# Optimization experiments

Measured on AMD Instinct MI355X. Metric: run time of the kernel, lower is better.

## Reference

```python
import jax, jax.numpy as jnp
import numpy as np

NUM_CLASSES = 91
BBOX_XFORM_CLIP = float(np.log(1000.0 / 16.0))
WX, WY, WW, WH = 10.0, 10.0, 5.0, 5.0  # torchvision BoxCoder weights
DETECTIONS_PER_IMG = 100


def _decode_boxes(reg, props):
    # reg: [P, 4*C], props: [P, 4] -> [P, C, 4]  (torchvision BoxCoder.decode)
    widths = props[:, 2] - props[:, 0]
    heights = props[:, 3] - props[:, 1]
    ctr_x = props[:, 0] + 0.5 * widths
    ctr_y = props[:, 1] + 0.5 * heights
    r = reg.reshape(reg.shape[0], -1, 4)
    dx = r[..., 0] / WX
    dy = r[..., 1] / WY
    dw = jnp.minimum(r[..., 2] / WW, BBOX_XFORM_CLIP)
    dh = jnp.minimum(r[..., 3] / WH, BBOX_XFORM_CLIP)
    pcx = dx * widths[:, None] + ctr_x[:, None]
    pcy = dy * heights[:, None] + ctr_y[:, None]
    pw = jnp.exp(dw) * widths[:, None]
    ph = jnp.exp(dh) * heights[:, None]
    return jnp.stack([pcx - 0.5 * pw, pcy - 0.5 * ph, pcx + 0.5 * pw, pcy + 0.5 * ph], axis=-1)


def _clip_boxes(boxes, h, w):
    x = jnp.clip(boxes[..., 0::2], 0.0, float(w))
    y = jnp.clip(boxes[..., 1::2], 0.0, float(h))
    return jnp.stack([x[..., 0], y[..., 0], x[..., 1], y[..., 1]], axis=-1)


def setup_inputs() -> dict:
    key = jax.random.key(0)
    k1, k2, k3, k4, k5 = jax.random.split(key, 5)
    B, P, C, FD = 8, 4096, NUM_CLASSES, 1024
    N = B * P
    class_logits = jax.random.normal(k1, (N, C), dtype=jnp.float32)
    box_regression = 0.5 * jax.random.normal(k2, (N, 4 * C), dtype=jnp.float32)
    # valid proposal boxes inside an 800x800 image: x1<x2, y1<y2
    xy = jax.random.uniform(k3, (N, 2), dtype=jnp.float32) * 700.0
    wh = jax.random.uniform(k4, (N, 2), dtype=jnp.float32) * 96.0 + 4.0
    proposals = jnp.concatenate([xy, xy + wh], axis=-1)
    box_features = jax.random.normal(k5, (N, FD), dtype=jnp.float32)
    return {"class_logits": class_logits, "box_regression": box_regression,
            "proposals": proposals, "box_features": box_features,
            "batch_size": B, "image_h": 800, "image_w": 800}


def reference(class_logits, box_regression, proposals, box_features, batch_size, image_h, image_w):
    B = int(batch_size)
    N = class_logits.shape[0]
    P = N // B
    lg = class_logits.reshape(B, P, NUM_CLASSES)
    rg = box_regression.reshape(B, P, 4 * NUM_CLASSES)
    pr = proposals.reshape(B, P, 4)
    ft = box_features.reshape(B, P, -1)

    def per_image(lg_i, rg_i, pr_i, ft_i):
        boxes = _decode_boxes(rg_i, pr_i)            # [P, C, 4]
        scores = jax.nn.softmax(lg_i, axis=-1)       # [P, C]
        boxes = _clip_boxes(boxes, image_h, image_w)
        boxes = boxes[:, 1:].reshape(-1, 4)          # drop background class -> [P*(C-1), 4]
        scores = scores[:, 1:].reshape(-1)
        # batched_nms with iou_threshold=1.0 never suppresses anything (IoU<=1 always),
        # so keep == indices sorted by score descending, truncated to detections_per_img.
        keep = jnp.argsort(-scores)[:DETECTIONS_PER_IMG]
        boxes = boxes / float(image_h)               # source divides by image_shape[0] only
        kept_boxes = boxes[keep]                     # [D, 4]
        feat_idx = keep // (NUM_CLASSES - 1)         # source: keep / (num_classes-1) int div
        kept_feats = ft_i[feat_idx]                  # [D, FD]
        return kept_boxes, kept_feats

    all_boxes, all_features = jax.vmap(per_image)(lg, rg, pr, ft)
    return all_boxes, all_features
```

## Files before the change

### kernel.cpp

```cpp
#include <hip/hip_runtime.h>
#include <hip/hip_bf16.h>

#define NCLS 91
#define NFG 90
#define NDET 100
#define FDIM 1024
#define CAP 4096
#define NBUK 4096
#define PMAX 4096
#define BBOX_CLIP 4.135166556742356f
#define K1_TPB 256
#define RPB 32
#define K2_TPB 1024

__global__ __launch_bounds__(K1_TPB) void k1_soft(
        const float* __restrict__ logits, float* __restrict__ rowoff,
        unsigned* __restrict__ maxk, int N) {
    int wave = threadIdx.x >> 6, lane = threadIdx.x & 63;
    int rowbase = blockIdx.x * RPB + wave * (RPB / 4);
    for (int it = 0; it < RPB / 4; it++) {
        long long row = rowbase + it;
        if (row >= N) return;
        const float* r = logits + row * NCLS;
        float l1 = r[lane];
        float l2 = (lane < NCLS - 64) ? r[64 + lane] : -INFINITY;
        float m = fmaxf(l1, l2);
        #pragma unroll
        for (int o = 32; o; o >>= 1) m = fmaxf(m, __shfl_xor(m, o));
        float e = expf(l1 - m) + ((lane < NCLS - 64) ? expf(l2 - m) : 0.0f);
        #pragma unroll
        for (int o = 32; o; o >>= 1) e += __shfl_xor(e, o);
        float off = m + logf(e);
        unsigned ka = (lane >= 1) ? __float_as_uint(expf(l1 - off)) : 0u;
        unsigned kb = (lane < NCLS - 64) ? __float_as_uint(expf(l2 - off)) : 0u;
        unsigned km = ka > kb ? ka : kb;
        #pragma unroll
        for (int o = 32; o; o >>= 1) { unsigned t = __shfl_xor(km, o); km = km > t ? km : t; }
        if (lane == 0) { rowoff[row] = off; maxk[row] = km; }
    }
}

__global__ __launch_bounds__(K2_TPB) void k2_select(
        const float* __restrict__ logits, const float* __restrict__ reg,
        const float* __restrict__ props,
        const int* __restrict__ pH, const int* __restrict__ pW,
        const float* __restrict__ rowoff, const unsigned* __restrict__ maxk,
        float* __restrict__ outBoxes, unsigned* __restrict__ keepRow, int P) {
    __shared__ unsigned long long cand[CAP];
    __shared__ unsigned hist[NBUK];
    __shared__ unsigned hot[PMAX];
    __shared__ unsigned tpart[256];
    __shared__ unsigned tsuf[257];
    __shared__ unsigned keepR[NDET];
    __shared__ unsigned sh_lb, sh_nhot, sh_ncand;

    const int img = blockIdx.x;
    const int tid = threadIdx.x;
    const unsigned* mk = maxk + (size_t)img * P;

    if (tid == 0) { sh_nhot = 0; sh_ncand = 0; sh_lb = 0; }
    for (int b = tid; b < NBUK; b += K2_TPB) hist[b] = 0u;
    __syncthreads();

    for (int r = tid; r < P; r += K2_TPB) atomicAdd(&hist[mk[r] >> 20], 1u);
    __syncthreads();

    unsigned local[16];
    if (tid < 256) {
        unsigned s = 0;
        #pragma unroll
        for (int i = 0; i < 16; i++) { local[i] = hist[tid * 16 + i]; s += local[i]; }
        tpart[tid] = s;
    }
    __syncthreads();
    if (tid == 0) {
        unsigned run = 0; tsuf[256] = 0;
        for (int t = 255; t >= 0; t--) { run += tpart[t]; tsuf[t] = run; }
    }
    __syncthreads();
    if (tid < 256) {
        unsigned run = tsuf[tid + 1];
        #pragma unroll
        for (int i = 15; i >= 0; i--) {
            unsigned prev = run; run += local[i];
            if (run >= NDET && prev < NDET) sh_lb = ((unsigned)(tid * 16 + i)) << 20;
        }
    }
    __syncthreads();
    const unsigned lb = sh_lb;

    for (int r = tid; r < P; r += K2_TPB)
        if (mk[r] >= lb) hot[atomicAdd(&sh_nhot, 1u)] = (unsigned)r;
    __syncthreads();
    const int nhot = (int)sh_nhot;

    const int wave = tid >> 6, lane = tid & 63;
    for (int i = wave; i < nhot; i += K2_TPB / 64) {
        int rl = (int)hot[i];
        long long row = (long long)img * P + rl;
        float off = rowoff[row];
        const float* r = logits + row * NCLS;
        float l1 = r[lane];
        float l2 = (lane < NCLS - 64) ? r[64 + lane] : -INFINITY;
        if (lane >= 1) {
            unsigned k = __float_as_uint(expf(l1 - off));
            if (k >= lb) {
                unsigned pos = atomicAdd(&sh_ncand, 1u);
                if (pos < CAP)
                    cand[pos] = ((unsigned long long)k << 32) |
                                (unsigned)(0xFFFFFFFFu - (unsigned)(rl * NFG + lane - 1));
            }
        }
        if (lane < NCLS - 64) {
            unsigned k = __float_as_uint(expf(l2 - off));
            if (k >= lb) {
                unsigned pos = atomicAdd(&sh_ncand, 1u);
                if (pos < CAP)
                    cand[pos] = ((unsigned long long)k << 32) |
                                (unsigned)(0xFFFFFFFFu - (unsigned)(rl * NFG + 63 + lane));
            }
        }
    }
    __syncthreads();
    unsigned cnt = sh_ncand; if (cnt > CAP) cnt = CAP;

    int n = 128; while (n < (int)cnt) n <<= 1;
    for (int i = tid; i < n; i += K2_TPB) if (i >= (int)cnt) cand[i] = 0ULL;
    __syncthreads();
    for (int k = 2; k <= n; k <<= 1) {
        for (int j = k >> 1; j > 0; j >>= 1) {
            for (int i = tid; i < n; i += K2_TPB) {
                int ixj = i ^ j;
                if (ixj > i) {
                    bool up = ((i & k) == 0);
                    unsigned long long a = cand[i], b = cand[ixj];
                    if ((a > b) == up) { cand[i] = b; cand[ixj] = a; }
                }
            }
            __syncthreads();
        }
    }

    if (tid < NDET) {
        unsigned long long key = cand[n - 1 - tid];
        unsigned e = 0xFFFFFFFFu - (unsigned)(key & 0xFFFFFFFFull);
        int pr = e / NFG, cm = e - pr * NFG, c = cm + 1;
        long long rw = (long long)img * P + pr;
        float x1 = props[rw * 4 + 0], y1 = props[rw * 4 + 1];
        float x2 = props[rw * 4 + 2], y2 = props[rw * 4 + 3];
        float w = x2 - x1, hgt = y2 - y1;
        float cx = x1 + 0.5f * w, cy = y1 + 0.5f * hgt;
        const float* rr = reg + rw * (4 * NCLS) + 4 * c;
        float dx = rr[0] / 10.0f, dy = rr[1] / 10.0f;
        float dw = fminf(rr[2] / 5.0f, BBOX_CLIP);
        float dh = fminf(rr[3] / 5.0f, BBOX_CLIP);
        float pcx = dx * w + cx, pcy = dy * hgt + cy;
        float pw_ = expf(dw) * w, ph_ = expf(dh) * hgt;
        float bx1 = pcx - 0.5f * pw_, by1 = pcy - 0.5f * ph_;
        float bx2 = pcx + 0.5f * pw_, by2 = pcy + 0.5f * ph_;
        float W = (float)(*pW), H = (float)(*pH);
        bx1 = fminf(fmaxf(bx1, 0.0f), W);
        bx2 = fminf(fmaxf(bx2, 0.0f), W);
        by1 = fminf(fmaxf(by1, 0.0f), H);
        by2 = fminf(fmaxf(by2, 0.0f), H);
        int o = (img * NDET + tid) * 4;
        outBoxes[o + 0] = bx1 / H;
        outBoxes[o + 1] = by1 / H;
        outBoxes[o + 2] = bx2 / H;
        outBoxes[o + 3] = by2 / H;
        keepRow[img * NDET + tid] = (unsigned)rw;
    }
}

__global__ __launch_bounds__(256) void k3_feats(
        const float* __restrict__ feats, const unsigned* __restrict__ keepRow,
        float* __restrict__ outF) {
    int det = blockIdx.x;
    long long r = keepRow[det];
    const float4* src = (const float4*)(feats + r * FDIM);
    float4* dst = (float4*)(outF + (long long)det * FDIM);
    dst[threadIdx.x] = src[threadIdx.x];
}

extern "C" void kernel_launch(void* const* d_in, const int* in_sizes, int n_in,
                              void* d_out, int out_size, void* d_ws, size_t ws_size,
                              hipStream_t stream) {
    const float* logits = (const float*)d_in[0];
    const float* reg    = (const float*)d_in[1];
    const float* props  = (const float*)d_in[2];
    const float* feats  = (const float*)d_in[3];
    const int*   pH     = (const int*)d_in[5];
    const int*   pW     = (const int*)d_in[6];

    int N = in_sizes[0] / NCLS;
    int B = out_size / (NDET * (4 + FDIM));
    int P = N / B;

    char* ws = (char*)d_ws;
    float*    rowoff  = (float*)ws;
    unsigned* maxk    = (unsigned*)(rowoff + N);
    unsigned* keepRow = (unsigned*)(maxk + N);

    float* outBoxes = (float*)d_out;
    float* outFeats = outBoxes + (size_t)B * NDET * 4;

    k1_soft<<<(N + RPB - 1) / RPB, K1_TPB, 0, stream>>>(logits, rowoff, maxk, N);
    k2_select<<<B, K2_TPB, 0, stream>>>(logits, reg, props, pH, pW,
                                        rowoff, maxk, outBoxes, keepRow, P);
    k3_feats<<<B * NDET, 256, 0, stream>>>(feats, keepRow, outFeats);
}
```

Baseline: 228.2 us.

## Add second-level radix refinement before bitonic sort and simplify row max

Candidates passing the coarse histogram threshold are re-bucketed on finer key bits (bits 52..63 of the packed key), and only those above a second threshold are copied into a smaller buffer, so the bitonic sort runs on far fewer elements. The threshold scan now uses wave shuffles instead of a serial single-thread suffix sum. The per-row max probability is derived from the foreground max logit rather than a second exp-and-reduce pass. This adds extra histogram passes and barriers, and it relies on the hot-row threshold being lowered by one to stay safe against exp rounding.

```diff
diff --git a/kernel.cpp b/kernel.cpp
--- a/kernel.cpp
+++ b/kernel.cpp
@@ -7,7 +7,6 @@
 #define FDIM 1024
 #define CAP 4096
 #define NBUK 4096
-#define PMAX 4096
 #define BBOX_CLIP 4.135166556742356f
 #define K1_TPB 256
 #define RPB 32
@@ -24,20 +23,48 @@
         const float* r = logits + row * NCLS;
         float l1 = r[lane];
         float l2 = (lane < NCLS - 64) ? r[64 + lane] : -INFINITY;
-        float m = fmaxf(l1, l2);
-        #pragma unroll
-        for (int o = 32; o; o >>= 1) m = fmaxf(m, __shfl_xor(m, o));
+        float mf = fmaxf((lane == 0) ? -INFINITY : l1, l2);
+        #pragma unroll
+        for (int o = 32; o; o >>= 1) mf = fmaxf(mf, __shfl_xor(mf, o));
+        float m = fmaxf(mf, __shfl(l1, 0));
         float e = expf(l1 - m) + ((lane < NCLS - 64) ? expf(l2 - m) : 0.0f);
         #pragma unroll
         for (int o = 32; o; o >>= 1) e += __shfl_xor(e, o);
         float off = m + logf(e);
-        unsigned ka = (lane >= 1) ? __float_as_uint(expf(l1 - off)) : 0u;
-        unsigned kb = (lane < NCLS - 64) ? __float_as_uint(expf(l2 - off)) : 0u;
-        unsigned km = ka > kb ? ka : kb;
-        #pragma unroll
-        for (int o = 32; o; o >>= 1) { unsigned t = __shfl_xor(km, o); km = km > t ? km : t; }
+        unsigned km = __float_as_uint(expf(mf - off));
         if (lane == 0) { rowoff[row] = off; maxk[row] = km; }
     }
+}
+
+__device__ __forceinline__ void find_threshold(const unsigned* hist,
+                                               unsigned* wsum, unsigned* sh_lb,
+                                               int tid, unsigned target) {
+    unsigned local[16]; unsigned s = 0, run = 0;
+    if (tid < 256) {
+        #pragma unroll
+        for (int i = 0; i < 16; i++) { local[i] = hist[tid * 16 + i]; s += local[i]; }
+        run = s;
+        #pragma unroll
+        for (int off = 1; off < 64; off <<= 1) {
+            unsigned v = __shfl_down(run, off);
+            if ((tid & 63) + off < 64) run += v;
+        }
+        if ((tid & 63) == 0) wsum[tid >> 6] = run;
+    }
+    __syncthreads();
+    if (tid < 256) {
+        int w = tid >> 6;
+        #pragma unroll
+        for (int ww = 0; ww < 4; ww++) if (ww > w) run += wsum[ww];
+        unsigned above = run - s;
+        #pragma unroll
+        for (int i = 15; i >= 0; i--) {
+            unsigned prev = above; above += local[i];
+            if (above >= target && prev < target)
+                *sh_lb = ((unsigned)(tid * 16 + i)) << 20;
+        }
+    }
+    __syncthreads();
 }
 
 __global__ __launch_bounds__(K2_TPB) void k2_select(
@@ -47,50 +74,28 @@
         const float* __restrict__ rowoff, const unsigned* __restrict__ maxk,
         float* __restrict__ outBoxes, unsigned* __restrict__ keepRow, int P) {
     __shared__ unsigned long long cand[CAP];
+    __shared__ unsigned long long cbuf[2048];
     __shared__ unsigned hist[NBUK];
-    __shared__ unsigned hot[PMAX];
-    __shared__ unsigned tpart[256];
-    __shared__ unsigned tsuf[257];
-    __shared__ unsigned keepR[NDET];
-    __shared__ unsigned sh_lb, sh_nhot, sh_ncand;
+    __shared__ unsigned wsum[4];
+    __shared__ unsigned sh_lb, sh_lb2, sh_nhot, sh_ncand, sh_n2;
 
     const int img = blockIdx.x;
     const int tid = threadIdx.x;
     const unsigned* mk = maxk + (size_t)img * P;
-
-    if (tid == 0) { sh_nhot = 0; sh_ncand = 0; sh_lb = 0; }
+    unsigned* hot = (unsigned*)cbuf;
+
+    if (tid == 0) { sh_nhot = 0; sh_ncand = 0; sh_n2 = 0; sh_lb = 0; sh_lb2 = 0; }
     for (int b = tid; b < NBUK; b += K2_TPB) hist[b] = 0u;
     __syncthreads();
 
     for (int r = tid; r < P; r += K2_TPB) atomicAdd(&hist[mk[r] >> 20], 1u);
     __syncthreads();
-
-    unsigned local[16];
-    if (tid < 256) {
-        unsigned s = 0;
-        #pragma unroll
-        for (int i = 0; i < 16; i++) { local[i] = hist[tid * 16 + i]; s += local[i]; }
-        tpart[tid] = s;
-    }
-    __syncthreads();
-    if (tid == 0) {
-        unsigned run = 0; tsuf[256] = 0;
-        for (int t = 255; t >= 0; t--) { run += tpart[t]; tsuf[t] = run; }
-    }
-    __syncthreads();
-    if (tid < 256) {
-        unsigned run = tsuf[tid + 1];
-        #pragma unroll
-        for (int i = 15; i >= 0; i--) {
-            unsigned prev = run; run += local[i];
-            if (run >= NDET && prev < NDET) sh_lb = ((unsigned)(tid * 16 + i)) << 20;
-        }
-    }
-    __syncthreads();
+    find_threshold(hist, wsum, &sh_lb, tid, NDET);
     const unsigned lb = sh_lb;
+    const unsigned lbh = lb ? lb - 1 : 0;
 
     for (int r = tid; r < P; r += K2_TPB)
-        if (mk[r] >= lb) hot[atomicAdd(&sh_nhot, 1u)] = (unsigned)r;
+        if (mk[r] >= lbh) hot[atomicAdd(&sh_nhot, 1u)] = (unsigned)r;
     __syncthreads();
     const int nhot = (int)sh_nhot;
 
@@ -123,10 +128,42 @@
     }
     __syncthreads();
     unsigned cnt = sh_ncand; if (cnt > CAP) cnt = CAP;
-
-    int n = 128; while (n < (int)cnt) n <<= 1;
-    for (int i = tid; i < n; i += K2_TPB) if (i >= (int)cnt) cand[i] = 0ULL;
-    __syncthreads();
+    int n;
+
+    if (cnt > 128) {
+        for (int b = tid; b < NBUK; b += K2_TPB) hist[b] = 0u;
+        __syncthreads();
+        for (int i = tid; i < (int)cnt; i += K2_TPB)
+            atomicAdd(&hist[(unsigned)(cand[i] >> 52)], 1u);
+        __syncthreads();
+        find_threshold(hist, wsum, &sh_lb2, tid, NDET);
+        unsigned lb2 = sh_lb2;
+        for (int i = tid; i < (int)cnt; i += K2_TPB) {
+            unsigned long long k64 = cand[i];
+            if ((unsigned)(k64 >> 32) >= lb2) {
+                unsigned pos = atomicAdd(&sh_n2, 1u);
+                if (pos < 2048) cbuf[pos] = k64;
+            }
+        }
+        __syncthreads();
+        unsigned cnt2 = sh_n2;
+        if (cnt2 <= 2048) {
+            cnt = cnt2;
+            n = 128; while (n < (int)cnt) n <<= 1;
+            for (int i = tid; i < n; i += K2_TPB)
+                cand[i] = (i < (int)cnt) ? cbuf[i] : 0ULL;
+            __syncthreads();
+        } else {
+            n = 128; while (n < (int)cnt) n <<= 1;
+            for (int i = tid; i < n; i += K2_TPB) if (i >= (int)cnt) cand[i] = 0ULL;
+            __syncthreads();
+        }
+    } else {
+        n = 128;
+        for (int i = tid; i < n; i += K2_TPB) if (i >= (int)cnt) cand[i] = 0ULL;
+        __syncthreads();
+    }
+
     for (int k = 2; k <= n; k <<= 1) {
         for (int j = k >> 1; j > 0; j >>= 1) {
             for (int i = tid; i < n; i += K2_TPB) {
```

After: 222.9 us. 1.02x faster.
